# Kernel tuning notes

Measured on AMD Instinct MI355X. Metric: run time of the kernel, lower is better.

The kernel has to match this reference:

```python
import jax, jax.numpy as jnp
import numpy as np

B, K, D = 131072, 4096, 64
COMMITMENT_COST = 0.25


def setup_inputs() -> dict:
    key = jax.random.key(0)
    k1, k2 = jax.random.split(key)
    inputs = jax.random.normal(k1, (B, D), dtype=jnp.float32)
    codebook = jax.random.normal(k2, (K, D), dtype=jnp.float32)
    return {"inputs": inputs, "codebook": codebook}


def reference(inputs, codebook):
    distances = (
        jnp.sum(inputs ** 2, axis=1, keepdims=True)
        + jnp.sum(codebook ** 2, axis=1)
        - 2.0 * jnp.matmul(inputs, codebook.T)
    )
    encoding_indices = jnp.argmin(distances, axis=1)  # (B,)
    quantized = codebook[encoding_indices]            # (B, D)
    sg = jax.lax.stop_gradient
    loss = (
        jnp.mean((sg(quantized) - inputs) ** 2)
        + COMMITMENT_COST * jnp.mean((quantized - sg(inputs)) ** 2)
    )
    # straight-through estimator
    quantized_st = inputs + sg(quantized - inputs)
    return quantized_st, loss
```

## Files before the change

kernel.cpp:

```cpp
#include <hip/hip_runtime.h>
#include <stdint.h>

constexpr int Bn = 131072, Kn = 4096, Dn = 64;
constexpr int NCHUNK = 256;
constexpr int HCHUNK = 128;
constexpr float TAU_S = 0.02f;

typedef short bf16x8 __attribute__((ext_vector_type(8)));
typedef float f32x4  __attribute__((ext_vector_type(4)));

__device__ __forceinline__ uint32_t rneb(float f) {
    uint32_t u = __float_as_uint(f);
    return (u + 0x7FFFu + ((u >> 16) & 1u)) >> 16;
}
__device__ __forceinline__ float bfval(uint32_t b) { return __uint_as_float(b << 16); }

struct Split8 { bf16x8 hi, lo; };
__device__ __forceinline__ Split8 split8(float4 a, float4 b) {
    uint32_t h0=rneb(a.x),h1=rneb(a.y),h2=rneb(a.z),h3=rneb(a.w);
    uint32_t h4=rneb(b.x),h5=rneb(b.y),h6=rneb(b.z),h7=rneb(b.w);
    uint32_t l0=rneb(a.x-bfval(h0)), l1=rneb(a.y-bfval(h1));
    uint32_t l2=rneb(a.z-bfval(h2)), l3=rneb(a.w-bfval(h3));
    uint32_t l4=rneb(b.x-bfval(h4)), l5=rneb(b.y-bfval(h5));
    uint32_t l6=rneb(b.z-bfval(h6)), l7=rneb(b.w-bfval(h7));
    union { bf16x8 v; uint32_t u[4]; } H, L;
    H.u[0]=h0|(h1<<16); H.u[1]=h2|(h3<<16); H.u[2]=h4|(h5<<16); H.u[3]=h6|(h7<<16);
    L.u[0]=l0|(l1<<16); L.u[1]=l2|(l3<<16); L.u[2]=l4|(l5<<16); L.u[3]=l6|(l7<<16);
    Split8 r; r.hi = H.v; r.lo = L.v; return r;
}

__global__ __launch_bounds__(256) void vq_prep(const float* __restrict__ cb,
                                               uint8_t* __restrict__ stage,
                                               float* __restrict__ negcn) {
    int t = blockIdx.x * 256 + threadIdx.x;
    int code = t >> 3, oct = t & 7;
    const float4* cp = (const float4*)(cb + (size_t)code * Dn + oct * 8);
    float4 f0 = cp[0], f1 = cp[1];
    Split8 s = split8(f0, f1);
    int j = code & 15, cc = code >> 4;
    uint8_t* base = stage + (size_t)cc * 4096;
    int dsto = (((oct & 3) * 16 + j) << 4) + ((oct & 4) ? 1024 : 0);
    *(bf16x8*)(base + dsto)        = s.hi;
    *(bf16x8*)(base + 2048 + dsto) = s.lo;
    float n = f0.x*f0.x + f0.y*f0.y + f0.z*f0.z + f0.w*f0.w
            + f1.x*f1.x + f1.y*f1.y + f1.z*f1.z + f1.w*f1.w;
    n += __shfl_xor(n, 1); n += __shfl_xor(n, 2); n += __shfl_xor(n, 4);
    if (oct == 0) negcn[code] = -0.5f * n;
}

__global__ void vq_zero(float* __restrict__ loss_acc, int* __restrict__ flag_cnt) {
    *loss_acc = 0.0f; *flag_cnt = 0;
}

__global__ __launch_bounds__(256, 3) void vq_main(
    const float* __restrict__ x, const uint8_t* __restrict__ stage,
    const float* __restrict__ negcn, const float* __restrict__ cb,
    float* __restrict__ out, float* __restrict__ loss_acc,
    int* __restrict__ flag_cnt, int* __restrict__ flag_rows) {

    __shared__ float sneg[Kn];
    __shared__ float smv1[4][64], smv2[4][64];
    __shared__ int   smk[4][64];
    __shared__ int   sres[128];

    const int tid = threadIdx.x;
    const int lane = tid & 63, w = tid >> 6;
    const int g = lane >> 4, j = lane & 15;
    const int kh = w & 1;
    const int cstart = kh * HCHUNK;

    #pragma unroll
    for (int i = 0; i < 16; ++i) sneg[i*256 + tid] = negcn[i*256 + tid];

    const int rowbase = blockIdx.x * 128 + (w >> 1) * 64;
    bf16x8 ah[4][2], al[4][2];
    #pragma unroll
    for (int t = 0; t < 4; ++t) {
        const float* xr = x + (size_t)(rowbase + t*16 + j) * Dn + g*8;
        Split8 s0 = split8(*(const float4*)xr,        *(const float4*)(xr + 4));
        Split8 s1 = split8(*(const float4*)(xr + 32), *(const float4*)(xr + 36));
        ah[t][0] = s0.hi; al[t][0] = s0.lo;
        ah[t][1] = s1.hi; al[t][1] = s1.lo;
    }

    float b1[16], b2[16];
    #pragma unroll
    for (int s = 0; s < 16; ++s) { b1[s] = -3.4e38f; b2[s] = -3.4e38f; }

    const uint8_t* sp = stage + (lane << 4);
    bf16x8 Bf[2][4];
    #pragma unroll
    for (int p = 0; p < 2; ++p) {
        const uint8_t* bbp = sp + ((size_t)(cstart + p) << 12);
        Bf[p][0] = *(const bf16x8*)(bbp);
        Bf[p][1] = *(const bf16x8*)(bbp + 1024);
        Bf[p][2] = *(const bf16x8*)(bbp + 2048);
        Bf[p][3] = *(const bf16x8*)(bbp + 3072);
    }
    __syncthreads();

#define TOP2(ACC, BASE)                                                       \
    _Pragma("unroll")                                                         \
    for (int q = 0; q < 4; ++q) {                                             \
        int s = (BASE) + q;                                                   \
        uint32_t vb = (__float_as_uint(ACC[q]) & 0xFFFFFF00u) | (uint32_t)c_; \
        float vp = __uint_as_float(vb);                                       \
        float ob1 = b1[s];                                                    \
        b2[s] = __builtin_amdgcn_fmed3f(vp, ob1, b2[s]);                      \
        b1[s] = fmaxf(ob1, vp);                                               \
    }

#define CHUNK_BODY(P, C, RELOAD)                                              \
    {                                                                         \
        const uint32_t c_ = (uint32_t)(C);                                    \
        bf16x8 B0 = Bf[P][0], B1 = Bf[P][1], B2 = Bf[P][2], B3 = Bf[P][3];    \
        float nc = sneg[((int)c_ << 4) + j];                                  \
        f32x4 a0 = {nc,nc,nc,nc}, a1 = {nc,nc,nc,nc};                         \
        f32x4 a2 = {nc,nc,nc,nc}, a3 = {nc,nc,nc,nc};                         \
        a0 = __builtin_amdgcn_mfma_f32_16x16x32_bf16(ah[0][0], B0, a0, 0,0,0);\
        a1 = __builtin_amdgcn_mfma_f32_16x16x32_bf16(ah[1][0], B0, a1, 0,0,0);\
        a2 = __builtin_amdgcn_mfma_f32_16x16x32_bf16(ah[2][0], B0, a2, 0,0,0);\
        a3 = __builtin_amdgcn_mfma_f32_16x16x32_bf16(ah[3][0], B0, a3, 0,0,0);\
        a0 = __builtin_amdgcn_mfma_f32_16x16x32_bf16(ah[0][1], B1, a0, 0,0,0);\
        a1 = __builtin_amdgcn_mfma_f32_16x16x32_bf16(ah[1][1], B1, a1, 0,0,0);\
        a2 = __builtin_amdgcn_mfma_f32_16x16x32_bf16(ah[2][1], B1, a2, 0,0,0);\
        a3 = __builtin_amdgcn_mfma_f32_16x16x32_bf16(ah[3][1], B1, a3, 0,0,0);\
        a0 = __builtin_amdgcn_mfma_f32_16x16x32_bf16(al[0][0], B0, a0, 0,0,0);\
        a1 = __builtin_amdgcn_mfma_f32_16x16x32_bf16(al[1][0], B0, a1, 0,0,0);\
        a2 = __builtin_amdgcn_mfma_f32_16x16x32_bf16(al[2][0], B0, a2, 0,0,0);\
        a3 = __builtin_amdgcn_mfma_f32_16x16x32_bf16(al[3][0], B0, a3, 0,0,0);\
        a0 = __builtin_amdgcn_mfma_f32_16x16x32_bf16(al[0][1], B1, a0, 0,0,0);\
        a1 = __builtin_amdgcn_mfma_f32_16x16x32_bf16(al[1][1], B1, a1, 0,0,0);\
        a2 = __builtin_amdgcn_mfma_f32_16x16x32_bf16(al[2][1], B1, a2, 0,0,0);\
        a3 = __builtin_amdgcn_mfma_f32_16x16x32_bf16(al[3][1], B1, a3, 0,0,0);\
        a0 = __builtin_amdgcn_mfma_f32_16x16x32_bf16(ah[0][0], B2, a0, 0,0,0);\
        a1 = __builtin_amdgcn_mfma_f32_16x16x32_bf16(ah[1][0], B2, a1, 0,0,0);\
        a2 = __builtin_amdgcn_mfma_f32_16x16x32_bf16(ah[2][0], B2, a2, 0,0,0);\
        a3 = __builtin_amdgcn_mfma_f32_16x16x32_bf16(ah[3][0], B2, a3, 0,0,0);\
        a0 = __builtin_amdgcn_mfma_f32_16x16x32_bf16(ah[0][1], B3, a0, 0,0,0);\
        a1 = __builtin_amdgcn_mfma_f32_16x16x32_bf16(ah[1][1], B3, a1, 0,0,0);\
        a2 = __builtin_amdgcn_mfma_f32_16x16x32_bf16(ah[2][1], B3, a2, 0,0,0);\
        a3 = __builtin_amdgcn_mfma_f32_16x16x32_bf16(ah[3][1], B3, a3, 0,0,0);\
        if (RELOAD) {                 \
            const uint8_t* nb = sp + ((size_t)(c_ + 2) << 12);                \
            Bf[P][0] = *(const bf16x8*)(nb);                                  \
            Bf[P][1] = *(const bf16x8*)(nb + 1024);                           \
            Bf[P][2] = *(const bf16x8*)(nb + 2048);                           \
            Bf[P][3] = *(const bf16x8*)(nb + 3072);                           \
        }                                                                     \
        TOP2(a0, 0) TOP2(a1, 4) TOP2(a2, 8) TOP2(a3, 12)                      \
    }

    #pragma unroll 1
    for (int c4 = cstart; c4 < cstart + HCHUNK - 2; c4 += 2) {
        CHUNK_BODY(0, c4 + 0, true)
        CHUNK_BODY(1, c4 + 1, true)
    }
    CHUNK_BODY(0, cstart + HCHUNK - 2, false)
    CHUNK_BODY(1, cstart + HCHUNK - 1, false)
#undef CHUNK_BODY
#undef TOP2

    #pragma unroll
    for (int s = 0; s < 16; ++s) {
        float v1 = b1[s], v2 = b2[s];
        int kk = (int)((__float_as_uint(v1) & 0xFFu) << 4) + j;
        #pragma unroll
        for (int m = 1; m < 16; m <<= 1) {
            float p1 = __shfl_xor(v1, m);
            float p2 = __shfl_xor(v2, m);
            int pk = __shfl_xor(kk, m);
            v2 = fmaxf(fmaxf(v2, p2), fminf(v1, p1));
            bool take = (p1 > v1) || ((p1 == v1) && (pk < kk));
            v1 = take ? p1 : v1;
            kk = take ? pk : kk;
        }
        if (j == 0) {
            int row = (s >> 2)*16 + g*4 + (s & 3);
            smv1[w][row] = v1; smv2[w][row] = v2; smk[w][row] = kk;
        }
    }
    __syncthreads();

    if (tid < 128) {
        int rt = tid >> 6, r = tid & 63;
        int wa = rt * 2, wb = wa + 1;
        float v1a = smv1[wa][r], v2a = smv2[wa][r];
        float v1b = smv1[wb][r], v2b = smv2[wb][r];
        int   ka  = smk[wa][r],  kb  = smk[wb][r];
        bool take = v1b > v1a;
        float m1 = take ? v1b : v1a;
        int   kk = take ? kb  : ka;
        float m2 = fmaxf(fmaxf(v2a, v2b), fminf(v1a, v1b));
        int flag = ((m1 - m2) < TAU_S) ? (int)0x80000000 : 0;
        sres[tid] = kk | flag;
    }
    __syncthreads();

    float ls = 0.f;
    const size_t blockrow = (size_t)blockIdx.x * 128;
    #pragma unroll 1
    for (int it = 0; it < 8; ++it) {
        int f = it * 256 + tid;
        int r = f >> 4, q = f & 15;
        int pk = sres[r];
        int idx = pk & 0x7FFFFFFF;
        bool flagged = pk < 0;
        size_t grow = blockrow + r;
        float4 xx = ((const float4*)(x + grow * Dn))[q];
        float4 qq = ((const float4*)(cb + (size_t)idx * Dn))[q];
        float dx = qq.x - xx.x, dy = qq.y - xx.y, dz = qq.z - xx.z, dw = qq.w - xx.w;
        float4 o; o.x = xx.x + dx; o.y = xx.y + dy; o.z = xx.z + dz; o.w = xx.w + dw;
        ((float4*)(out + grow * Dn))[q] = o;
        if (flagged) {
            if (q == 0) { int p = atomicAdd(flag_cnt, 1); flag_rows[p] = (int)grow; }
        } else {
            ls = fmaf(dx, dx, ls); ls = fmaf(dy, dy, ls);
            ls = fmaf(dz, dz, ls); ls = fmaf(dw, dw, ls);
        }
    }
    #pragma unroll
    for (int m = 1; m < 64; m <<= 1) ls += __shfl_xor(ls, m);
    if (lane == 0) atomicAdd(loss_acc, ls);
}

__global__ __launch_bounds__(256) void vq_cleanup(
    const float* __restrict__ x, const float* __restrict__ cb,
    const int* __restrict__ flag_cnt, const int* __restrict__ flag_rows,
    float* __restrict__ out, float* __restrict__ loss_acc) {
    __shared__ double sxd[4][Dn];
    __shared__ double swb[4][4];
    __shared__ int    swi[4][4];
    const int tid = threadIdx.x;
    const int n = *flag_cnt;

    for (int it = blockIdx.x; it * 4 < n; it += gridDim.x) {
        const int base = it * 4;
        const int nr = min(4, n - base);
        __syncthreads();
        {
            int rr = tid >> 6, e = tid & 63;
            int row = flag_rows[base + ((rr < nr) ? rr : 0)];
            sxd[rr][e] = (double)x[(size_t)row * Dn + e];
        }
        __syncthreads();

        double best[4]; int bidx[4];
        #pragma unroll
        for (int r2 = 0; r2 < 4; ++r2) { best[r2] = 1.0e300; bidx[r2] = 0x7FFFFFFF; }

        #pragma unroll 1
        for (int i = 0; i < Kn / 256; ++i) {
            const int k = i * 256 + tid;
            const float* c4 = cb + (size_t)k * Dn;
            double cn = 0.0;
            double d0 = 0.0, d1 = 0.0, d2 = 0.0, d3 = 0.0;
            #pragma unroll 8
            for (int e = 0; e < Dn; ++e) {
                double ce = (double)c4[e];
                cn = fma(ce, ce, cn);
                d0 = fma(ce, sxd[0][e], d0);
                d1 = fma(ce, sxd[1][e], d1);
                d2 = fma(ce, sxd[2][e], d2);
                d3 = fma(ce, sxd[3][e], d3);
            }
            double dd[4] = { cn - 2.0*d0, cn - 2.0*d1, cn - 2.0*d2, cn - 2.0*d3 };
            #pragma unroll
            for (int r2 = 0; r2 < 4; ++r2)
                if (dd[r2] < best[r2] || (dd[r2] == best[r2] && k < bidx[r2])) {
                    best[r2] = dd[r2]; bidx[r2] = k;
                }
        }
        #pragma unroll
        for (int r2 = 0; r2 < 4; ++r2) {
            double bb = best[r2]; int bi = bidx[r2];
            #pragma unroll
            for (int m = 1; m < 64; m <<= 1) {
                double pb = __shfl_xor(bb, m);
                int    pi = __shfl_xor(bi, m);
                if (pb < bb || (pb == bb && pi < bi)) { bb = pb; bi = pi; }
            }
            if ((tid & 63) == 0) { swb[r2][tid >> 6] = bb; swi[r2][tid >> 6] = bi; }
        }
        __syncthreads();
        if (tid < 4) {
            double fb = swb[tid][0]; int fi = swi[tid][0];
            #pragma unroll
            for (int wv = 1; wv < 4; ++wv) {
                double pb = swb[tid][wv]; int pi = swi[tid][wv];
                if (pb < fb || (pb == fb && pi < fi)) { fb = pb; fi = pi; }
            }
            swi[tid][0] = fi;
        }
        __syncthreads();

        if (tid < 64) {
            int r2 = tid >> 4, q = tid & 15;
            if (r2 < nr) {
                int row = flag_rows[base + r2];
                int fi  = swi[r2][0];
                float4 xx = ((const float4*)(x + (size_t)row * Dn))[q];
                float4 qq = ((const float4*)(cb + (size_t)fi * Dn))[q];
                float dx = qq.x - xx.x, dy = qq.y - xx.y, dz = qq.z - xx.z, dw = qq.w - xx.w;
                float4 o; o.x = xx.x + dx; o.y = xx.y + dy; o.z = xx.z + dz; o.w = xx.w + dw;
                ((float4*)(out + (size_t)row * Dn))[q] = o;
                float ls = dx*dx + dy*dy + dz*dz + dw*dw;
                ls += __shfl_xor(ls, 1); ls += __shfl_xor(ls, 2);
                ls += __shfl_xor(ls, 4); ls += __shfl_xor(ls, 8);
                if (q == 0) atomicAdd(loss_acc, ls);
            }
        }
    }
}

__global__ void vq_final(float* __restrict__ loss_acc) {
    *loss_acc = *loss_acc * (1.25f / (float)(Bn * Dn));
}

extern "C" void kernel_launch(void* const* d_in, const int* in_sizes, int n_in,
                              void* d_out, int out_size, void* d_ws, size_t ws_size,
                              hipStream_t stream) {
    const float* x  = (const float*)d_in[0];
    const float* cb = (const float*)d_in[1];
    float* out  = (float*)d_out;
    float* loss = out + (size_t)Bn * Dn;

    uint8_t* wsb = (uint8_t*)d_ws;
    float*   negcn     = (float*)wsb;
    uint8_t* stage     = wsb + 16384;
    int*     flag_cnt  = (int*)(wsb + 16384 + (size_t)NCHUNK * 4096);
    int*     flag_rows = flag_cnt + 1;

    vq_prep<<<128, 256, 0, stream>>>(cb, stage, negcn);
    vq_zero<<<1, 1, 0, stream>>>(loss, flag_cnt);
    vq_main<<<Bn / 128, 256, 0, stream>>>(x, stage, negcn, cb, out, loss, flag_cnt, flag_rows);
    vq_cleanup<<<512, 256, 0, stream>>>(x, cb, flag_cnt, flag_rows, out, loss);
    vq_final<<<1, 1, 0, stream>>>(loss);
}
```

Baseline: 263.6 us.

## Fold codebook norm bias into an extra MFMA and widen cleanup to eight rows

The -0.5*|c|^2 bias is split into bf16 hi/lo and stored in an extra 1KB slice of each staged codebook chunk. It is injected through one additional MFMA against a constant ones vector, which replaces the shared-memory norm table, its per-block fill and the block barrier. The cost is one more MFMA and one more 16-byte load per chunk per lane, plus some bias precision loss that the cleanup pass must absorb. The fp64 cleanup kernel now handles eight flagged rows per iteration instead of four, to reuse each codebook read across more rows at the price of more registers.

```diff
diff --git a/kernel.cpp b/kernel.cpp
--- a/kernel.cpp
+++ b/kernel.cpp
@@ -4,6 +4,7 @@
 constexpr int Bn = 131072, Kn = 4096, Dn = 64;
 constexpr int NCHUNK = 256;
 constexpr int HCHUNK = 128;
+constexpr int CBYTES = 5120;
 constexpr float TAU_S = 0.02f;
 
 typedef short bf16x8 __attribute__((ext_vector_type(8)));
@@ -30,22 +31,30 @@
 }
 
 __global__ __launch_bounds__(256) void vq_prep(const float* __restrict__ cb,
-                                               uint8_t* __restrict__ stage,
-                                               float* __restrict__ negcn) {
+                                               uint8_t* __restrict__ stage) {
     int t = blockIdx.x * 256 + threadIdx.x;
     int code = t >> 3, oct = t & 7;
     const float4* cp = (const float4*)(cb + (size_t)code * Dn + oct * 8);
     float4 f0 = cp[0], f1 = cp[1];
     Split8 s = split8(f0, f1);
     int j = code & 15, cc = code >> 4;
-    uint8_t* base = stage + (size_t)cc * 4096;
+    uint8_t* base = stage + (size_t)cc * CBYTES;
     int dsto = (((oct & 3) * 16 + j) << 4) + ((oct & 4) ? 1024 : 0);
     *(bf16x8*)(base + dsto)        = s.hi;
     *(bf16x8*)(base + 2048 + dsto) = s.lo;
     float n = f0.x*f0.x + f0.y*f0.y + f0.z*f0.z + f0.w*f0.w
             + f1.x*f1.x + f1.y*f1.y + f1.z*f1.z + f1.w*f1.w;
     n += __shfl_xor(n, 1); n += __shfl_xor(n, 2); n += __shfl_xor(n, 4);
-    if (oct == 0) negcn[code] = -0.5f * n;
+    if (oct == 0) {
+        float nn = -0.5f * n;
+        uint32_t nh = rneb(nn);
+        uint32_t nl = rneb(nn - bfval(nh));
+        uint4 z = { nh | (nl << 16), 0u, 0u, 0u };
+        *(uint4*)(base + 4096 + j * 16) = z;
+    } else if (oct <= 3) {
+        uint4 z = { 0u, 0u, 0u, 0u };
+        *(uint4*)(base + 4096 + oct * 256 + j * 16) = z;
+    }
 }
 
 __global__ void vq_zero(float* __restrict__ loss_acc, int* __restrict__ flag_cnt) {
@@ -54,11 +63,10 @@
 
 __global__ __launch_bounds__(256, 3) void vq_main(
     const float* __restrict__ x, const uint8_t* __restrict__ stage,
-    const float* __restrict__ negcn, const float* __restrict__ cb,
-    float* __restrict__ out, float* __restrict__ loss_acc,
-    int* __restrict__ flag_cnt, int* __restrict__ flag_rows) {
-
-    __shared__ float sneg[Kn];
+    const float* __restrict__ cb, float* __restrict__ out,
+    float* __restrict__ loss_acc, int* __restrict__ flag_cnt,
+    int* __restrict__ flag_rows) {
+
     __shared__ float smv1[4][64], smv2[4][64];
     __shared__ int   smk[4][64];
     __shared__ int   sres[128];
@@ -68,9 +76,6 @@
     const int g = lane >> 4, j = lane & 15;
     const int kh = w & 1;
     const int cstart = kh * HCHUNK;
-
-    #pragma unroll
-    for (int i = 0; i < 16; ++i) sneg[i*256 + tid] = negcn[i*256 + tid];
 
     const int rowbase = blockIdx.x * 128 + (w >> 1) * 64;
     bf16x8 ah[4][2], al[4][2];
@@ -83,27 +88,36 @@
         ah[t][1] = s1.hi; al[t][1] = s1.lo;
     }
 
+    bf16x8 acst;
+    {
+        union { bf16x8 v; uint32_t u[4]; } A;
+        A.u[0] = (lane < 16) ? 0x3F803F80u : 0u;
+        A.u[1] = 0u; A.u[2] = 0u; A.u[3] = 0u;
+        acst = A.v;
+    }
+    const f32x4 zero4 = {0.f, 0.f, 0.f, 0.f};
+
     float b1[16], b2[16];
     #pragma unroll
     for (int s = 0; s < 16; ++s) { b1[s] = -3.4e38f; b2[s] = -3.4e38f; }
 
     const uint8_t* sp = stage + (lane << 4);
-    bf16x8 Bf[2][4];
+    bf16x8 Bf[2][5];
     #pragma unroll
     for (int p = 0; p < 2; ++p) {
-        const uint8_t* bbp = sp + ((size_t)(cstart + p) << 12);
+        const uint8_t* bbp = sp + (size_t)(cstart + p) * CBYTES;
         Bf[p][0] = *(const bf16x8*)(bbp);
         Bf[p][1] = *(const bf16x8*)(bbp + 1024);
         Bf[p][2] = *(const bf16x8*)(bbp + 2048);
         Bf[p][3] = *(const bf16x8*)(bbp + 3072);
-    }
-    __syncthreads();
+        Bf[p][4] = *(const bf16x8*)(bbp + 4096);
+    }
 
 #define TOP2(ACC, BASE)                                                       \
     _Pragma("unroll")                                                         \
     for (int q = 0; q < 4; ++q) {                                             \
         int s = (BASE) + q;                                                   \
-        uint32_t vb = (__float_as_uint(ACC[q]) & 0xFFFFFF00u) | (uint32_t)c_; \
+        uint32_t vb = (__float_as_uint(ACC[q]) & 0xFFFFFF00u) | c_;           \
         float vp = __uint_as_float(vb);                                       \
         float ob1 = b1[s];                                                    \
         b2[s] = __builtin_amdgcn_fmed3f(vp, ob1, b2[s]);                      \
@@ -114,13 +128,13 @@
     {                                                                         \
         const uint32_t c_ = (uint32_t)(C);                                    \
         bf16x8 B0 = Bf[P][0], B1 = Bf[P][1], B2 = Bf[P][2], B3 = Bf[P][3];    \
-        float nc = sneg[((int)c_ << 4) + j];                                  \
-        f32x4 a0 = {nc,nc,nc,nc}, a1 = {nc,nc,nc,nc};                         \
-        f32x4 a2 = {nc,nc,nc,nc}, a3 = {nc,nc,nc,nc};                         \
-        a0 = __builtin_amdgcn_mfma_f32_16x16x32_bf16(ah[0][0], B0, a0, 0,0,0);\
-        a1 = __builtin_amdgcn_mfma_f32_16x16x32_bf16(ah[1][0], B0, a1, 0,0,0);\
-        a2 = __builtin_amdgcn_mfma_f32_16x16x32_bf16(ah[2][0], B0, a2, 0,0,0);\
-        a3 = __builtin_amdgcn_mfma_f32_16x16x32_bf16(ah[3][0], B0, a3, 0,0,0);\
+        bf16x8 B4 = Bf[P][4];                                                 \
+          \
+        f32x4 nacc = __builtin_amdgcn_mfma_f32_16x16x32_bf16(acst, B4, zero4, 0,0,0); \
+        f32x4 a0 = __builtin_amdgcn_mfma_f32_16x16x32_bf16(ah[0][0], B0, nacc, 0,0,0);\
+        f32x4 a1 = __builtin_amdgcn_mfma_f32_16x16x32_bf16(ah[1][0], B0, nacc, 0,0,0);\
+        f32x4 a2 = __builtin_amdgcn_mfma_f32_16x16x32_bf16(ah[2][0], B0, nacc, 0,0,0);\
+        f32x4 a3 = __builtin_amdgcn_mfma_f32_16x16x32_bf16(ah[3][0], B0, nacc, 0,0,0);\
         a0 = __builtin_amdgcn_mfma_f32_16x16x32_bf16(ah[0][1], B1, a0, 0,0,0);\
         a1 = __builtin_amdgcn_mfma_f32_16x16x32_bf16(ah[1][1], B1, a1, 0,0,0);\
         a2 = __builtin_amdgcn_mfma_f32_16x16x32_bf16(ah[2][1], B1, a2, 0,0,0);\
@@ -142,11 +156,12 @@
         a2 = __builtin_amdgcn_mfma_f32_16x16x32_bf16(ah[2][1], B3, a2, 0,0,0);\
         a3 = __builtin_amdgcn_mfma_f32_16x16x32_bf16(ah[3][1], B3, a3, 0,0,0);\
         if (RELOAD) {                 \
-            const uint8_t* nb = sp + ((size_t)(c_ + 2) << 12);                \
+            const uint8_t* nb = sp + (size_t)(c_ + 2) * CBYTES;               \
             Bf[P][0] = *(const bf16x8*)(nb);                                  \
             Bf[P][1] = *(const bf16x8*)(nb + 1024);                           \
             Bf[P][2] = *(const bf16x8*)(nb + 2048);                           \
             Bf[P][3] = *(const bf16x8*)(nb + 3072);                           \
+            Bf[P][4] = *(const bf16x8*)(nb + 4096);                           \
         }                                                                     \
         TOP2(a0, 0) TOP2(a1, 4) TOP2(a2, 8) TOP2(a3, 12)                      \
     }
@@ -228,33 +243,34 @@
     const float* __restrict__ x, const float* __restrict__ cb,
     const int* __restrict__ flag_cnt, const int* __restrict__ flag_rows,
     float* __restrict__ out, float* __restrict__ loss_acc) {
-    __shared__ double sxd[4][Dn];
-    __shared__ double swb[4][4];
-    __shared__ int    swi[4][4];
+    __shared__ double sxd[8][Dn];
+    __shared__ double swb[8][4];
+    __shared__ int    swi[8][4];
     const int tid = threadIdx.x;
     const int n = *flag_cnt;
 
-    for (int it = blockIdx.x; it * 4 < n; it += gridDim.x) {
-        const int base = it * 4;
-        const int nr = min(4, n - base);
+    for (int it = blockIdx.x; it * 8 < n; it += gridDim.x) {
+        const int base = it * 8;
+        const int nr = min(8, n - base);
         __syncthreads();
         {
-            int rr = tid >> 6, e = tid & 63;
+            int rr = tid >> 5, e = tid & 31;
             int row = flag_rows[base + ((rr < nr) ? rr : 0)];
-            sxd[rr][e] = (double)x[(size_t)row * Dn + e];
+            sxd[rr][e]      = (double)x[(size_t)row * Dn + e];
+            sxd[rr][e + 32] = (double)x[(size_t)row * Dn + e + 32];
         }
         __syncthreads();
 
-        double best[4]; int bidx[4];
+        double best[8]; int bidx[8];
         #pragma unroll
-        for (int r2 = 0; r2 < 4; ++r2) { best[r2] = 1.0e300; bidx[r2] = 0x7FFFFFFF; }
+        for (int r2 = 0; r2 < 8; ++r2) { best[r2] = 1.0e300; bidx[r2] = 0x7FFFFFFF; }
 
         #pragma unroll 1
         for (int i = 0; i < Kn / 256; ++i) {
             const int k = i * 256 + tid;
             const float* c4 = cb + (size_t)k * Dn;
             double cn = 0.0;
-            double d0 = 0.0, d1 = 0.0, d2 = 0.0, d3 = 0.0;
+            double d0=0.0,d1=0.0,d2=0.0,d3=0.0,d4=0.0,d5=0.0,d6=0.0,d7=0.0;
             #pragma unroll 8
             for (int e = 0; e < Dn; ++e) {
                 double ce = (double)c4[e];
@@ -263,16 +279,21 @@
                 d1 = fma(ce, sxd[1][e], d1);
                 d2 = fma(ce, sxd[2][e], d2);
                 d3 = fma(ce, sxd[3][e], d3);
+                d4 = fma(ce, sxd[4][e], d4);
+                d5 = fma(ce, sxd[5][e], d5);
+                d6 = fma(ce, sxd[6][e], d6);
+                d7 = fma(ce, sxd[7][e], d7);
             }
-            double dd[4] = { cn - 2.0*d0, cn - 2.0*d1, cn - 2.0*d2, cn - 2.0*d3 };
+            double dd[8] = { cn - 2.0*d0, cn - 2.0*d1, cn - 2.0*d2, cn - 2.0*d3,
+                             cn - 2.0*d4, cn - 2.0*d5, cn - 2.0*d6, cn - 2.0*d7 };
             #pragma unroll
-            for (int r2 = 0; r2 < 4; ++r2)
+            for (int r2 = 0; r2 < 8; ++r2)
                 if (dd[r2] < best[r2] || (dd[r2] == best[r2] && k < bidx[r2])) {
                     best[r2] = dd[r2]; bidx[r2] = k;
                 }
         }
         #pragma unroll
-        for (int r2 = 0; r2 < 4; ++r2) {
+        for (int r2 = 0; r2 < 8; ++r2) {
             double bb = best[r2]; int bi = bidx[r2];
             #pragma unroll
             for (int m = 1; m < 64; m <<= 1) {
@@ -283,7 +304,7 @@
             if ((tid & 63) == 0) { swb[r2][tid >> 6] = bb; swi[r2][tid >> 6] = bi; }
         }
         __syncthreads();
-        if (tid < 4) {
+        if (tid < 8) {
             double fb = swb[tid][0]; int fi = swi[tid][0];
             #pragma unroll
             for (int wv = 1; wv < 4; ++wv) {
@@ -294,7 +315,7 @@
         }
         __syncthreads();
 
-        if (tid < 64) {
+        if (tid < 128) {
             int r2 = tid >> 4, q = tid & 15;
             if (r2 < nr) {
                 int row = flag_rows[base + r2];
@@ -326,14 +347,13 @@
     float* loss = out + (size_t)Bn * Dn;
 
     uint8_t* wsb = (uint8_t*)d_ws;
-    float*   negcn     = (float*)wsb;
-    uint8_t* stage     = wsb + 16384;
-    int*     flag_cnt  = (int*)(wsb + 16384 + (size_t)NCHUNK * 4096);
+    uint8_t* stage     = wsb;
+    int*     flag_cnt  = (int*)(wsb + (size_t)NCHUNK * CBYTES);
     int*     flag_rows = flag_cnt + 1;
 
-    vq_prep<<<128, 256, 0, stream>>>(cb, stage, negcn);
+    vq_prep<<<128, 256, 0, stream>>>(cb, stage);
     vq_zero<<<1, 1, 0, stream>>>(loss, flag_cnt);
-    vq_main<<<Bn / 128, 256, 0, stream>>>(x, stage, negcn, cb, out, loss, flag_cnt, flag_rows);
+    vq_main<<<Bn / 128, 256, 0, stream>>>(x, stage, cb, out, loss, flag_cnt, flag_rows);
     vq_cleanup<<<512, 256, 0, stream>>>(x, cb, flag_cnt, flag_rows, out, loss);
     vq_final<<<1, 1, 0, stream>>>(loss);
 }
```

Result: slower. 819.6 us (+210.9%).
